# Performance work log

Hardware: AMD Instinct MI355X
Metric: run time of the kernel (lower is better)

The kernel has to match this reference:

```python
import jax, jax.numpy as jnp
import numpy as np
from jax import lax

CHUNK = 64          # rows per chunk in the parabola pass (bounds peak memory)
INF = jnp.float32(1e12)  # 'no site in this column' sentinel for squared distance


def _edt_sq(mask):
    """Exact squared Euclidean distance transform of a 2D bool mask.

    Matches scipy.ndimage.distance_transform_edt(mask)**2: for pixels where
    mask is True (nonzero), squared distance to the nearest False (zero)
    pixel; 0 at False pixels. Separable: 1D along-column distance, then a
    brute-force lower-envelope (parabola) pass along rows, which is exact.
    """
    h, w = mask.shape
    sites = ~mask  # zero pixels = distance sources
    idx = jnp.arange(h, dtype=jnp.int32)[:, None]  # [H,1]
    # distance (in rows) to nearest site above / below in the same column
    up = idx - lax.cummax(jnp.where(sites, idx, -h), axis=0)
    down = lax.cummin(jnp.where(sites, idx, 2 * h), axis=0, reverse=True) - idx
    d = jnp.minimum(up, down)  # >= h means no site in this column
    g = jnp.where(d >= h, INF, d.astype(jnp.float32) ** 2)  # [H,W]

    # parabola pass along axis 1: out[r, j] = min_k g[r, k] + (j-k)^2
    j = jnp.arange(w, dtype=jnp.float32)
    dk2 = (j[:, None] - j[None, :]) ** 2  # [W_j, W_k]

    def row_chunk(gc):  # gc: [CHUNK, W]
        return jnp.min(gc[:, None, :] + dk2[None, :, :], axis=-1)

    gch = g.reshape(h // CHUNK, CHUNK, w)
    return lax.map(row_chunk, gch).reshape(h, w)


def _signed_distance(t):
    """t: bool foreground mask. Returns inside*(~t) - (outside-1)*t, where
    outside = EDT(t) (fg pixel -> nearest bg) and inside = EDT(~t)
    (bg pixel -> nearest fg), as in the original distance_metric."""
    outside = jnp.sqrt(_edt_sq(t))
    inside = jnp.sqrt(_edt_sq(~t))
    tf = t.astype(jnp.float32)
    return inside * (1.0 - tf) - (outside - 1.0) * tf


def setup_inputs() -> dict:
    key = jax.random.key(0)
    k1, k2 = jax.random.split(key)
    inp = jax.random.normal(k1, (1024, 1024), dtype=jnp.float32)
    target = jax.random.randint(k2, (1024, 1024), 0, 2, dtype=jnp.int32)
    return {"input": inp, "target": target}


def reference(input, target):
    sd = _signed_distance(target != 0)
    return jnp.mean(input * sd)
```

## Files before the change

### kernel.cpp

```cpp
#include <hip/hip_runtime.h>

#define H 1024
#define W 1024
#define NPIX (H * W)
#define INF_F 1e12f
#define THREADS 256
#define NBLK (NPIX / THREADS)
#define RHALO 32

__global__ __launch_bounds__(THREADS) void edt_vertical(
    const int* __restrict__ target,
    float* __restrict__ g_t,
    float* __restrict__ g_nt) {
  int idx = blockIdx.x * THREADS + threadIdx.x;
  int r = idx >> 10;
  int t0 = target[idx];
  int dz = (t0 == 0) ? 0 : -1;
  int dn = (t0 != 0) ? 0 : -1;
  for (int base = 1; (dz | dn) < 0 && base < H; base += 4) {
#pragma unroll
    for (int u = 0; u < 4; ++u) {
      int dk = base + u;
      int vu = (r >= dk) ? target[idx - dk * W] : -1;
      int vd = (r + dk < H) ? target[idx + dk * W] : -1;
      if (dz < 0 && (vu == 0 || vd == 0)) dz = dk;
      if (dn < 0 && (vu > 0 || vd > 0)) dn = dk;
    }
  }
  g_t[idx]  = (dz < 0) ? INF_F : (float)(dz * dz);
  g_nt[idx] = (dn < 0) ? INF_F : (float)(dn * dn);
}

__global__ __launch_bounds__(THREADS) void edt_horiz(
    const int* __restrict__ target,
    const float* __restrict__ input,
    const float* __restrict__ g_t,
    const float* __restrict__ g_nt,
    double* __restrict__ partials) {
  __shared__ float sg2[2][THREADS + 2 * RHALO];
  const int tid = threadIdx.x;
  const int idx = blockIdx.x * THREADS + tid;
  const int j = idx & (W - 1);
  const int row0 = idx & ~(W - 1);
  const int cstart = (blockIdx.x * THREADS) & (W - 1);

  for (int e = tid; e < THREADS + 2 * RHALO; e += THREADS) {
    int c = cstart - RHALO + e;
    bool ok = (c >= 0) && (c < W);
    int gi = row0 + (ok ? c : 0);
    sg2[0][e] = ok ? g_t[gi] : INF_F;
    sg2[1][e] = ok ? g_nt[gi] : INF_F;
  }
  __syncthreads();

  const bool t = target[idx] != 0;
  const float* __restrict__ sg = &sg2[t ? 0 : 1][0];
  const int lj = tid + RHALO;

  float best = sg[lj];
  for (int base = 1; base + 3 <= RHALO; base += 4) {
    if ((float)(base * base) >= best) break;
#pragma unroll
    for (int u = 0; u < 4; ++u) {
      int dk = base + u;
      float dk2 = (float)(dk * dk);
      best = fminf(best, sg[lj - dk] + dk2);
      best = fminf(best, sg[lj + dk] + dk2);
    }
  }
  if ((float)((RHALO + 1) * (RHALO + 1)) < best) {
    const float* __restrict__ g = t ? g_t : g_nt;
    for (int dk = RHALO + 1; dk < W; ++dk) {
      float dk2 = (float)(dk * dk);
      if (dk2 >= best) break;
      if (j - dk >= 0) best = fminf(best, g[row0 + j - dk] + dk2);
      if (j + dk < W)  best = fminf(best, g[row0 + j + dk] + dk2);
    }
  }

  float dist = sqrtf(best);
  float sd = t ? (1.0f - dist) : dist;
  double val = (double)(input[idx] * sd);

  for (int off = 32; off > 0; off >>= 1)
    val += __shfl_down(val, off, 64);
  __shared__ double smem[THREADS / 64];
  int lane = tid & 63, wid = tid >> 6;
  if (lane == 0) smem[wid] = val;
  __syncthreads();
  if (tid == 0)
    partials[blockIdx.x] = smem[0] + smem[1] + smem[2] + smem[3];
}

__global__ __launch_bounds__(THREADS) void reduce_partials(
    const double* __restrict__ partials, float* __restrict__ out) {
  double s = 0.0;
  for (int i = threadIdx.x; i < NBLK; i += THREADS) s += partials[i];
  for (int off = 32; off > 0; off >>= 1)
    s += __shfl_down(s, off, 64);
  __shared__ double smem[THREADS / 64];
  int lane = threadIdx.x & 63, wid = threadIdx.x >> 6;
  if (lane == 0) smem[wid] = s;
  __syncthreads();
  if (threadIdx.x == 0)
    out[0] = (float)((smem[0] + smem[1] + smem[2] + smem[3]) / (double)NPIX);
}

extern "C" void kernel_launch(void* const* d_in, const int* in_sizes, int n_in,
                              void* d_out, int out_size, void* d_ws, size_t ws_size,
                              hipStream_t stream) {
  const float* input = (const float*)d_in[0];
  const int* target = (const int*)d_in[1];
  float* out = (float*)d_out;

  double* partials = (double*)d_ws;
  float* g_t = (float*)((char*)d_ws + 32 * 1024);
  float* g_nt = g_t + NPIX;

  edt_vertical<<<NBLK, THREADS, 0, stream>>>(target, g_t, g_nt);
  edt_horiz<<<NBLK, THREADS, 0, stream>>>(target, input, g_t, g_nt, partials);
  reduce_partials<<<1, THREADS, 0, stream>>>(partials, out);
}
```

Before: 77.35 us.

## Bit-pack target columns and fuse vertical and horizontal EDT into one kernel

Packs the target mask into 64-bit column words, then computes vertical distances with bit scans (clz/ctz) inside a fused kernel that handles 4 rows by 4 columns per thread. Per-pixel vertical distances are stored as bytes in shared memory for the horizontal pass, and exact fallbacks cover long distances. This removes the two full-size float g buffers and the per-pixel column scans over int data, cutting global memory traffic. It adds branchy fallback paths and fewer blocks (256), which may lower occupancy.

```diff
diff --git a/kernel.cpp b/kernel.cpp
--- a/kernel.cpp
+++ b/kernel.cpp
@@ -3,84 +3,173 @@
 #define H 1024
 #define W 1024
 #define NPIX (H * W)
+#define WW 16
 #define INF_F 1e12f
 #define THREADS 256
-#define NBLK (NPIX / THREADS)
-#define RHALO 32
-
-__global__ __launch_bounds__(THREADS) void edt_vertical(
-    const int* __restrict__ target,
-    float* __restrict__ g_t,
-    float* __restrict__ g_nt) {
-  int idx = blockIdx.x * THREADS + threadIdx.x;
-  int r = idx >> 10;
-  int t0 = target[idx];
-  int dz = (t0 == 0) ? 0 : -1;
-  int dn = (t0 != 0) ? 0 : -1;
-  for (int base = 1; (dz | dn) < 0 && base < H; base += 4) {
-#pragma unroll
-    for (int u = 0; u < 4; ++u) {
-      int dk = base + u;
-      int vu = (r >= dk) ? target[idx - dk * W] : -1;
-      int vd = (r + dk < H) ? target[idx + dk * W] : -1;
-      if (dz < 0 && (vu == 0 || vd == 0)) dz = dk;
-      if (dn < 0 && (vu > 0 || vd > 0)) dn = dk;
-    }
-  }
-  g_t[idx]  = (dz < 0) ? INF_F : (float)(dz * dz);
-  g_nt[idx] = (dn < 0) ? INF_F : (float)(dn * dn);
-}
-
-__global__ __launch_bounds__(THREADS) void edt_horiz(
-    const int* __restrict__ target,
+#define BIG (1 << 29)
+
+__device__ __noinline__ int vert_dist_full(const unsigned long long* __restrict__ pw,
+                                           int r, int c, int pol) {
+  int w = r >> 6, b = r & 63;
+  unsigned long long v = pw[w * W + c];
+  unsigned long long m_c = pol ? v : ~v;
+  int dup = 1 << 30, ddn = 1 << 30;
+  unsigned long long am = m_c & ((1ULL << b) - 1ULL);
+  if (am) {
+    dup = b - (63 - __builtin_clzll(am));
+  } else {
+    for (int ww = w - 1; ww >= 0; --ww) {
+      unsigned long long mv = pw[ww * W + c];
+      mv = pol ? mv : ~mv;
+      if (mv) { dup = r - (ww * 64 + 63 - __builtin_clzll(mv)); break; }
+    }
+  }
+  unsigned long long bm = m_c >> b;
+  if (bm) {
+    ddn = __builtin_ctzll(bm);
+  } else {
+    for (int ww = w + 1; ww < WW; ++ww) {
+      unsigned long long mv = pw[ww * W + c];
+      mv = pol ? mv : ~mv;
+      if (mv) { ddn = (ww * 64 + __builtin_ctzll(mv)) - r; break; }
+    }
+  }
+  return min(dup, ddn);
+}
+
+__device__ __noinline__ int horiz_exact(const unsigned long long* __restrict__ pw,
+                                        int r, int c, int pol, int best, int dk0) {
+  for (int dk = dk0; dk < W; ++dk) {
+    int dk2 = dk * dk;
+    if (dk2 >= best) break;
+    if (c - dk >= 0) {
+      int d = vert_dist_full(pw, r, c - dk, pol);
+      if (d < H) best = min(best, d * d + dk2);
+    }
+    if (c + dk < W) {
+      int d = vert_dist_full(pw, r, c + dk, pol);
+      if (d < H) best = min(best, d * d + dk2);
+    }
+  }
+  return best;
+}
+
+__global__ __launch_bounds__(THREADS) void pack_bits(
+    const int* __restrict__ target, unsigned int* __restrict__ pw32) {
+  int tg = blockIdx.x * THREADS + threadIdx.x;
+  int w = tg >> 11;
+  int half = (tg >> 10) & 1;
+  int c = tg & (W - 1);
+  int rbase = w * 64 + half * 32;
+  unsigned int val = 0;
+#pragma unroll
+  for (int b = 0; b < 32; ++b) {
+    if (target[(rbase + b) * W + c] != 0) val |= (1u << b);
+  }
+  pw32[((w * W + c) << 1) + half] = val;
+}
+
+__global__ __launch_bounds__(THREADS) void fused_edt(
+    const unsigned long long* __restrict__ pw,
     const float* __restrict__ input,
-    const float* __restrict__ g_t,
-    const float* __restrict__ g_nt,
     double* __restrict__ partials) {
-  __shared__ float sg2[2][THREADS + 2 * RHALO];
+  __shared__ unsigned char sd8[8][W + 64];
   const int tid = threadIdx.x;
-  const int idx = blockIdx.x * THREADS + tid;
-  const int j = idx & (W - 1);
-  const int row0 = idx & ~(W - 1);
-  const int cstart = (blockIdx.x * THREADS) & (W - 1);
-
-  for (int e = tid; e < THREADS + 2 * RHALO; e += THREADS) {
-    int c = cstart - RHALO + e;
-    bool ok = (c >= 0) && (c < W);
-    int gi = row0 + (ok ? c : 0);
-    sg2[0][e] = ok ? g_t[gi] : INF_F;
-    sg2[1][e] = ok ? g_nt[gi] : INF_F;
-  }
+  const int r0 = blockIdx.x << 2;
+  const int w = r0 >> 6, b0 = r0 & 63;
+  const int c0 = tid << 2;
+
+  if (tid < 128) {
+    int p = tid >> 4, q = tid & 15;
+    ((unsigned int*)sd8)[p * 272 + (q < 8 ? q : 256 + q)] = 0xFFFFFFFFu;
+  }
+
+  unsigned long long curv[4], prevv[4], nextv[4];
+  *(ulonglong2*)&curv[0] = *(const ulonglong2*)(pw + w * W + c0);
+  *(ulonglong2*)&curv[2] = *(const ulonglong2*)(pw + w * W + c0 + 2);
+  const bool hp = (w > 0), hn = (w < WW - 1);
+  if (hp) {
+    *(ulonglong2*)&prevv[0] = *(const ulonglong2*)(pw + (w - 1) * W + c0);
+    *(ulonglong2*)&prevv[2] = *(const ulonglong2*)(pw + (w - 1) * W + c0 + 2);
+  } else prevv[0] = prevv[1] = prevv[2] = prevv[3] = 0ULL;
+  if (hn) {
+    *(ulonglong2*)&nextv[0] = *(const ulonglong2*)(pw + (w + 1) * W + c0);
+    *(ulonglong2*)&nextv[2] = *(const ulonglong2*)(pw + (w + 1) * W + c0 + 2);
+  } else nextv[0] = nextv[1] = nextv[2] = nextv[3] = 0ULL;
+
+  unsigned char dloc[2][4][4];
+#pragma unroll
+  for (int pol = 0; pol < 2; ++pol) {
+#pragma unroll
+    for (int k = 0; k < 4; ++k) {
+      unsigned long long m_c = pol ? curv[k] : ~curv[k];
+      unsigned long long m_p = hp ? (pol ? prevv[k] : ~prevv[k]) : 0ULL;
+      unsigned long long m_n = hn ? (pol ? nextv[k] : ~nextv[k]) : 0ULL;
+#pragma unroll
+      for (int rr = 0; rr < 4; ++rr) {
+        int b = b0 + rr;
+        int d = 1 << 30;
+        unsigned long long am = m_c & ((1ULL << b) - 1ULL);
+        if (am) d = b - (63 - __builtin_clzll(am));
+        else if (m_p) d = b + 1 + __builtin_clzll(m_p);
+        unsigned long long bm = m_c >> b;
+        int dd = 1 << 30;
+        if (bm) dd = __builtin_ctzll(bm);
+        else if (m_n) dd = (64 - b) + __builtin_ctzll(m_n);
+        d = min(d, dd);
+        if (d > 64) d = vert_dist_full(pw, r0 + rr, c0 + k, pol);
+        dloc[pol][rr][k] = (unsigned char)min(d, 255);
+      }
+    }
+  }
+#pragma unroll
+  for (int pol = 0; pol < 2; ++pol)
+#pragma unroll
+    for (int rr = 0; rr < 4; ++rr) {
+      unsigned int u = (unsigned int)dloc[pol][rr][0] |
+                       ((unsigned int)dloc[pol][rr][1] << 8) |
+                       ((unsigned int)dloc[pol][rr][2] << 16) |
+                       ((unsigned int)dloc[pol][rr][3] << 24);
+      *(unsigned int*)&sd8[pol * 4 + rr][32 + c0] = u;
+    }
   __syncthreads();
 
-  const bool t = target[idx] != 0;
-  const float* __restrict__ sg = &sg2[t ? 0 : 1][0];
-  const int lj = tid + RHALO;
-
-  float best = sg[lj];
-  for (int base = 1; base + 3 <= RHALO; base += 4) {
-    if ((float)(base * base) >= best) break;
-#pragma unroll
-    for (int u = 0; u < 4; ++u) {
-      int dk = base + u;
-      float dk2 = (float)(dk * dk);
-      best = fminf(best, sg[lj - dk] + dk2);
-      best = fminf(best, sg[lj + dk] + dk2);
-    }
-  }
-  if ((float)((RHALO + 1) * (RHALO + 1)) < best) {
-    const float* __restrict__ g = t ? g_t : g_nt;
-    for (int dk = RHALO + 1; dk < W; ++dk) {
-      float dk2 = (float)(dk * dk);
-      if (dk2 >= best) break;
-      if (j - dk >= 0) best = fminf(best, g[row0 + j - dk] + dk2);
-      if (j + dk < W)  best = fminf(best, g[row0 + j + dk] + dk2);
-    }
-  }
-
-  float dist = sqrtf(best);
-  float sd = t ? (1.0f - dist) : dist;
-  double val = (double)(input[idx] * sd);
+  double val = 0.0;
+#pragma unroll
+  for (int rr = 0; rr < 4; ++rr) {
+    const float4 iv = *(const float4*)(input + (r0 + rr) * W + c0);
+    const float ivk[4] = {iv.x, iv.y, iv.z, iv.w};
+#pragma unroll
+    for (int k = 0; k < 4; ++k) {
+      const bool t = (dloc[1][rr][k] == 0);
+      const int pol = t ? 0 : 1;
+      const int own = t ? dloc[0][rr][k] : dloc[1][rr][k];
+      int best = (own == 255) ? BIG : own * own;
+      const unsigned char* __restrict__ sg = &sd8[pol * 4 + rr][32 + c0 + k];
+      for (int dk = 1; dk <= 32; ++dk) {
+        int dk2 = dk * dk;
+        if (dk2 >= best) break;
+        int dl = sg[-dk], dr = sg[dk];
+        int gl = (dl == 255) ? BIG : dl * dl;
+        int gr = (dr == 255) ? BIG : dr * dr;
+        best = min(best, min(gl, gr) + dk2);
+      }
+      if (best > 1089) {
+        int r = r0 + rr, c = c0 + k;
+        if (best > 65025) {
+          int ov = vert_dist_full(pw, r, c, pol);
+          best = (ov < H) ? ov * ov : (1 << 30);
+          best = horiz_exact(pw, r, c, pol, best, 1);
+        } else {
+          best = horiz_exact(pw, r, c, pol, best, 33);
+        }
+      }
+      float bestf = (best >= BIG) ? INF_F : (float)best;
+      float dist = sqrtf(bestf);
+      float sd = t ? (1.0f - dist) : dist;
+      val += (double)(ivk[k] * sd);
+    }
+  }
 
   for (int off = 32; off > 0; off >>= 1)
     val += __shfl_down(val, off, 64);
@@ -94,8 +183,7 @@
 
 __global__ __launch_bounds__(THREADS) void reduce_partials(
     const double* __restrict__ partials, float* __restrict__ out) {
-  double s = 0.0;
-  for (int i = threadIdx.x; i < NBLK; i += THREADS) s += partials[i];
+  double s = partials[threadIdx.x];
   for (int off = 32; off > 0; off >>= 1)
     s += __shfl_down(s, off, 64);
   __shared__ double smem[THREADS / 64];
@@ -114,10 +202,9 @@
   float* out = (float*)d_out;
 
   double* partials = (double*)d_ws;
-  float* g_t = (float*)((char*)d_ws + 32 * 1024);
-  float* g_nt = g_t + NPIX;
-
-  edt_vertical<<<NBLK, THREADS, 0, stream>>>(target, g_t, g_nt);
-  edt_horiz<<<NBLK, THREADS, 0, stream>>>(target, input, g_t, g_nt, partials);
+  unsigned long long* pw = (unsigned long long*)((char*)d_ws + 4096);
+
+  pack_bits<<<128, THREADS, 0, stream>>>(target, (unsigned int*)pw);
+  fused_edt<<<H / 4, THREADS, 0, stream>>>(pw, input, partials);
   reduce_partials<<<1, THREADS, 0, stream>>>(partials, out);
 }
```

Result: faster. 69.59 us (-10.0%).
